# Kernel optimization log

Measured on AMD Instinct MI355X. Metric: run time of the kernel, lower is better.

The kernel has to match this reference:

```python
import jax, jax.numpy as jnp
import numpy as np

B, N, E = 4, 4096, 1024
H, D = 16, 64          # num_heads, head_dim
K = 256                # proj_dim
MAXN = 4096
RANK = 32


def setup_inputs() -> dict:
    key = jax.random.key(0)
    ks = jax.random.split(key, 9)
    def w(k, shape, fan_in):
        return jax.random.normal(k, shape, jnp.float32) * (1.0 / np.sqrt(fan_in))
    return {
        "x": jax.random.normal(ks[0], (B, N, E), jnp.float32),
        "qU": w(ks[1], (RANK, E), E),            # LowRankLinear U: [rank, in]
        "qV": w(ks[2], (E // 2, RANK), RANK),    # LowRankLinear V: [out, rank]
        "qW": w(ks[3], (H * D, E // 2), E // 2), # final query Linear weight
        "qb": jnp.zeros((H * D,), jnp.float32),
        "kW": w(ks[4], (D, E), E),               # key_transform (single kv head)
        "key_proj": w(ks[5], (MAXN, K), MAXN),   # Linformer projection [max_seq_len, proj_dim]
        "oW": w(ks[6], (E, H * D), H * D),
        "ob": jnp.zeros((E,), jnp.float32),
    }


def reference(x, qU, qV, qW, qb, kW, key_proj, oW, ob):
    b, n, _ = x.shape
    # query: LowRankLinear then Linear
    q = ((x @ qU.T) @ qV.T) @ qW.T + qb              # [b, n, H*D]
    # shared single-head key/value, projected along sequence to K slots
    k = x @ kW.T                                     # [b, n, D]
    kv = jnp.einsum('bnd,nk->bkd', k, key_proj[:n])  # [b, K, D]
    q = q.reshape(b, n, H, D).transpose(0, 2, 1, 3)  # [b, H, n, D]
    kv = kv[:, None]                                 # [b, 1, K, D] broadcasts over heads
    scores = jnp.einsum('bhnd,bhkd->bhnk', q, kv) * (D ** -0.5)
    w = jax.nn.softmax(scores, axis=-1)              # [b, H, n, K]
    out = jnp.einsum('bhnk,bhkd->bhnd', w, kv)       # [b, H, n, D]
    out = out.transpose(0, 2, 1, 3).reshape(b, n, H * D)
    return out @ oW.T + ob
```

## Files before the change

### kernel.cpp

```cpp
#include <hip/hip_runtime.h>


typedef unsigned short u16;
typedef _Float16 f16;
typedef __attribute__((ext_vector_type(8))) _Float16 h8;
typedef __attribute__((ext_vector_type(4))) float f32x4;
typedef __attribute__((ext_vector_type(8))) unsigned short us8;
typedef __attribute__((ext_vector_type(4))) unsigned short us4;

__device__ __forceinline__ u16 f2h(float x) {
    f16 h = (f16)x;
    union { f16 hf; u16 u; } c; c.hf = h; return c.u;
}
__device__ __forceinline__ void async16(const void* g, void* l) {
    __builtin_amdgcn_global_load_lds(
        (const __attribute__((address_space(1))) void*)g,
        (__attribute__((address_space(3))) void*)l, 16, 0, 0);
}

__global__ __launch_bounds__(256)
void cvt_w(const float* __restrict__ src, u16* __restrict__ h, int n4) {
    int i = blockIdx.x * 256 + threadIdx.x;
    if (i >= n4) return;
    float4 v = ((const float4*)src)[i];
    u16 hh[4] = {f2h(v.x), f2h(v.y), f2h(v.z), f2h(v.w)};
    ((us4*)h)[i] = *(const us4*)hh;
}

__global__ __launch_bounds__(256)
void wc_compute(const float* __restrict__ qW, const float* __restrict__ qV,
                u16* __restrict__ Wc) {
    __shared__ float Vs[128][32];
    const int t = threadIdx.x;
    const int nl = t >> 3;
    const int rg = t & 7;
    const int n0 = blockIdx.x * 32;
    float acc[4] = {0.f, 0.f, 0.f, 0.f};
    for (int e0 = 0; e0 < 512; e0 += 128) {
#pragma unroll
        for (int u = 0; u < 16; ++u) {
            int idx = u * 256 + t;
            int ee = idx >> 5, rr = idx & 31;
            Vs[ee][rr] = qV[(size_t)(e0 + ee) * 32 + rr];
        }
        __syncthreads();
        for (int e = 0; e < 128; ++e) {
            float w = qW[(size_t)(n0 + nl) * 512 + e0 + e];
#pragma unroll
            for (int rr = 0; rr < 4; ++rr)
                acc[rr] += w * Vs[e][rg * 4 + rr];
        }
        __syncthreads();
    }
#pragma unroll
    for (int rr = 0; rr < 4; ++rr)
        Wc[(size_t)(n0 + nl) * 32 + rg * 4 + rr] = f2h(acc[rr]);
}

template <bool HAS_BIAS, bool OUT_F16>
__global__ __launch_bounds__(256)
void gemm_ps(const u16* __restrict__ A_g, const u16* __restrict__ B_g,
             const float* __restrict__ bias, void* __restrict__ C_p,
             int M, int N, int K) {
    __shared__ u16 LA[128 * 32], LB[128 * 32];
    const int t = threadIdx.x;
    const int wave = t >> 6, lane = t & 63;
    const int l15 = lane & 15, quad = lane >> 4;
    const int wm = (wave >> 1) * 64, wn = (wave & 1) * 64;
    const int gx = gridDim.x;
    const int nwg = gx * gridDim.y;
    const int flat = blockIdx.y * gx + blockIdx.x;
    const int cpx = nwg >> 3;
    const int swz = (flat & 7) * cpx + (flat >> 3);
    const int m0 = (swz / gx) * 128, n0 = (swz % gx) * 128;
    const int rl = lane >> 2, c4 = lane & 3;

    f32x4 acc[4][4] = {};

    for (int k0 = 0; k0 < K; k0 += 32) {
#pragma unroll
        for (int j = 0; j < 2; ++j) {
            const int rloc = (wave * 2 + j) * 16 + rl;
            const size_t ga = (size_t)(m0 + rloc) * K + k0 + c4 * 8;
            const size_t gb = (size_t)(n0 + rloc) * K + k0 + c4 * 8;
            const int lo = (wave * 2 + j) * 512;
            async16(&A_g[ga], &LA[lo]);
            async16(&B_g[gb], &LB[lo]);
        }
        __syncthreads();

        h8 ah[4], bh[4];
#pragma unroll
        for (int i = 0; i < 4; ++i) {
            ah[i] = *(const h8*)&LA[(wm + i * 16 + l15) * 32 + quad * 8];
            bh[i] = *(const h8*)&LB[(wn + i * 16 + l15) * 32 + quad * 8];
        }
#pragma unroll
        for (int i = 0; i < 4; ++i)
#pragma unroll
            for (int j = 0; j < 4; ++j)
                acc[i][j] = __builtin_amdgcn_mfma_f32_16x16x32_f16(ah[i], bh[j], acc[i][j], 0, 0, 0);
        __syncthreads();
    }

#pragma unroll
    for (int j = 0; j < 4; ++j) {
        const int col = n0 + wn + j * 16 + l15;
        const float badd = HAS_BIAS ? bias[col] : 0.f;
#pragma unroll
        for (int i = 0; i < 4; ++i) {
            const int rbase = m0 + wm + i * 16 + quad * 4;
#pragma unroll
            for (int r = 0; r < 4; ++r) {
                float v = acc[i][j][r] + badd;
                size_t idx = (size_t)(rbase + r) * N + col;
                if (OUT_F16) ((u16*)C_p)[idx] = f2h(v);
                else         ((float*)C_p)[idx] = v;
            }
        }
    }
}

__global__ __launch_bounds__(256)
void gemm_x96(const float* __restrict__ A, const u16* __restrict__ B_g,
              u16* __restrict__ t1, float* __restrict__ km, int K) {
    __shared__ u16 Ah[64][40], Bh[96][40];
    const int t = threadIdx.x;
    const int wave = t >> 6, lane = t & 63;
    const int l15 = lane & 15, quad = lane >> 4;
    const int wm = wave * 16;
    const int m0 = blockIdx.y * 64;
    const int arow = t >> 2, acol = (t & 3) * 8;

    f32x4 acc[6] = {};

    for (int k0 = 0; k0 < K; k0 += 32) {
        {
            const float* src = &A[(size_t)(m0 + arow) * K + k0 + acol];
            float4 w0 = ((const float4*)src)[0], w1 = ((const float4*)src)[1];
            float v[8] = {w0.x, w0.y, w0.z, w0.w, w1.x, w1.y, w1.z, w1.w};
            u16 hh[8];
#pragma unroll
            for (int e = 0; e < 8; ++e) hh[e] = f2h(v[e]);
            *(us8*)&Ah[arow][acol] = *(const us8*)&hh[0];
        }
        if (t < 192) {
            const int brow = t >> 1, bcol = (t & 1) * 16;
            size_t base = (size_t)brow * K + k0 + bcol;
            *(us8*)&Bh[brow][bcol]     = *(const us8*)&B_g[base];
            *(us8*)&Bh[brow][bcol + 8] = *(const us8*)&B_g[base + 8];
        }
        __syncthreads();

        h8 ah = *(const h8*)&Ah[wm + l15][quad * 8];
        h8 bh[6];
#pragma unroll
        for (int j = 0; j < 6; ++j)
            bh[j] = *(const h8*)&Bh[j * 16 + l15][quad * 8];
#pragma unroll
        for (int j = 0; j < 6; ++j)
            acc[j] = __builtin_amdgcn_mfma_f32_16x16x32_f16(ah, bh[j], acc[j], 0, 0, 0);
        __syncthreads();
    }

#pragma unroll
    for (int j = 0; j < 6; ++j) {
        const int col96 = j * 16 + l15;
        const int rbase = m0 + wm + quad * 4;
#pragma unroll
        for (int r = 0; r < 4; ++r) {
            float v = acc[j][r];
            const int row = rbase + r;
            if (col96 < 32) t1[(size_t)row * 32 + col96] = f2h(v);
            else            km[(size_t)row * 64 + (col96 - 32)] = v;
        }
    }
}

__global__ __launch_bounds__(256)
void kv_partial(const float* __restrict__ kmat, const float* __restrict__ kp,
                float* __restrict__ part) {
    const int b = blockIdx.y;
    const int seg = blockIdx.z;
    const int kk0 = blockIdx.x * 16;
    const int tid = threadIdx.x;
    const int d = tid & 63, s = tid >> 6;

    float acc[16] = {};
    const int nbeg = seg * 512;
    for (int n = nbeg + s; n < nbeg + 512; n += 4) {
        const float kval = kmat[((size_t)b * 4096 + n) * 64 + d];
        const float* kpr = &kp[(size_t)n * 256 + kk0];
#pragma unroll
        for (int j = 0; j < 16; ++j) acc[j] += kval * kpr[j];
    }
    __shared__ float sm[16][4][64];
#pragma unroll
    for (int j = 0; j < 16; ++j) sm[j][s][d] = acc[j];
    __syncthreads();
    for (int o = tid; o < 16 * 64; o += 256) {
        const int j = o >> 6, dd = o & 63;
        part[(((size_t)seg * 4 + b) * 256 + kk0 + j) * 64 + dd] =
            sm[j][0][dd] + sm[j][1][dd] + sm[j][2][dd] + sm[j][3][dd];
    }
}

__global__ __launch_bounds__(256)
void kv_reduce_cvt(const float* __restrict__ part,
                   u16* __restrict__ kvh, u16* __restrict__ kvTh) {
    const int i = blockIdx.x * 256 + threadIdx.x;
    float s = 0.f;
#pragma unroll
    for (int seg = 0; seg < 8; ++seg) s += part[(size_t)seg * 65536 + i];
    u16 hh = f2h(s);
    kvh[i] = hh;
    const int b = i >> 14, k = (i >> 6) & 255, d = i & 63;
    kvTh[((size_t)b * 64 + d) * 256 + k] = hh;
}

__global__ __launch_bounds__(256)
void attn_fused(const u16* __restrict__ qh,
                const u16* __restrict__ kvh, const u16* __restrict__ kvTh,
                u16* __restrict__ ath) {
    __shared__ u16 Kh_s[64][72];
    __shared__ u16 Vh_s[64][72];
    __shared__ u16 Ps[128 * 64];
    const int b = blockIdx.z, h = blockIdx.y;
    const int t = threadIdx.x, wave = t >> 6, lane = t & 63;
    const int l15 = lane & 15, quad = lane >> 4;
    const int nblk = blockIdx.x * 128;
    const int nwav = wave * 32;
    char* Pb = (char*)Ps;

    h8 Qf[2][2];
#pragma unroll
    for (int nt = 0; nt < 2; ++nt) {
        size_t qoff = ((size_t)(b * 4096 + nblk + nwav + nt * 16 + l15)) * 1024
                      + h * 64 + quad * 8;
#pragma unroll
        for (int c = 0; c < 2; ++c)
            Qf[nt][c] = *(const h8*)&qh[qoff + c * 32];
    }

    f32x4 O[2][4] = {};
    float rsum[2] = {0.f, 0.f};

    const int srow = t >> 3;
    const int scol = (t & 7) * 8;
    const size_t kb = (size_t)b * 16384;

    for (int kc = 0; kc < 4; ++kc) {
        {
            us8 s0 = *(const us8*)&kvh [kb + (size_t)(kc * 64 + srow     ) * 64 + scol];
            us8 s1 = *(const us8*)&kvh [kb + (size_t)(kc * 64 + srow + 32) * 64 + scol];
            us8 s4 = *(const us8*)&kvTh[kb + (size_t)(srow     ) * 256 + kc * 64 + scol];
            us8 s5 = *(const us8*)&kvTh[kb + (size_t)(srow + 32) * 256 + kc * 64 + scol];
            *(us8*)&Kh_s[srow     ][scol] = s0;
            *(us8*)&Kh_s[srow + 32][scol] = s1;
            *(us8*)&Vh_s[srow     ][scol] = s4;
            *(us8*)&Vh_s[srow + 32][scol] = s5;
        }
        __syncthreads();

        f32x4 S[2][4] = {};
#pragma unroll
        for (int ktl = 0; ktl < 4; ++ktl) {
            const int krl = ktl * 16 + l15;
#pragma unroll
            for (int c = 0; c < 2; ++c) {
                h8 Kf = *(const h8*)&Kh_s[krl][c * 32 + quad * 8];
#pragma unroll
                for (int nt = 0; nt < 2; ++nt)
                    S[nt][ktl] = __builtin_amdgcn_mfma_f32_16x16x32_f16(Kf, Qf[nt][c], S[nt][ktl], 0, 0, 0);
            }
        }
#pragma unroll
        for (int nt = 0; nt < 2; ++nt) {
            const int nrel = nwav + nt * 16 + l15;
#pragma unroll
            for (int ktl = 0; ktl < 4; ++ktl) {
                u16 pw[4];
#pragma unroll
                for (int r = 0; r < 4; ++r) {
                    float p = __expf(S[nt][ktl][r] * 0.125f - 4.0f);
                    rsum[nt] += p;
                    pw[r] = f2h(p);
                }
                *(us4*)(Pb + ((nrel * 128 + ktl * 32 + quad * 8) ^ ((nrel & 7) << 4)))
                    = *(const us4*)pw;
            }
        }

#pragma unroll
        for (int c = 0; c < 2; ++c) {
            h8 pf[2];
#pragma unroll
            for (int nt = 0; nt < 2; ++nt) {
                const int nrel = nwav + nt * 16 + l15;
                pf[nt] = *(const h8*)(Pb + ((nrel * 128 + c * 64 + quad * 16) ^ ((nrel & 7) << 4)));
            }
#pragma unroll
            for (int dt = 0; dt < 4; ++dt) {
                const int drow = dt * 16 + l15;
                h8 th = *(const h8*)&Vh_s[drow][c * 32 + quad * 8];
#pragma unroll
                for (int nt = 0; nt < 2; ++nt)
                    O[nt][dt] = __builtin_amdgcn_mfma_f32_16x16x32_f16(pf[nt], th, O[nt][dt], 0, 0, 0);
            }
        }
        __syncthreads();
    }

    float inv[2];
#pragma unroll
    for (int nt = 0; nt < 2; ++nt) {
        float s = rsum[nt];
        s += __shfl_xor(s, 16, 64);
        s += __shfl_xor(s, 32, 64);
        inv[nt] = 1.f / s;
    }

#pragma unroll
    for (int nt = 0; nt < 2; ++nt)
#pragma unroll
        for (int dt = 0; dt < 4; ++dt) {
            const int dcol = dt * 16 + l15;
#pragma unroll
            for (int r = 0; r < 4; ++r) {
                const float qinv = __shfl(inv[nt], quad * 4 + r, 16);
                const int query = nblk + nwav + nt * 16 + quad * 4 + r;
                float v = O[nt][dt][r] * qinv;
                size_t idx = (size_t)(b * 4096 + query) * 1024 + h * 64 + dcol;
                ath[idx] = f2h(v);
            }
        }
}

extern "C" void kernel_launch(void* const* d_in, const int* in_sizes, int n_in,
                              void* d_out, int out_size, void* d_ws, size_t ws_size,
                              hipStream_t stream) {
    const float* x  = (const float*)d_in[0];
    const float* qU = (const float*)d_in[1];
    const float* qV = (const float*)d_in[2];
    const float* qW = (const float*)d_in[3];
    const float* qb = (const float*)d_in[4];
    const float* kW = (const float*)d_in[5];
    const float* kp = (const float*)d_in[6];
    const float* oW = (const float*)d_in[7];
    const float* ob = (const float*)d_in[8];
    float* out = (float*)d_out;

    const int M = 16384;
    u16* W = (u16*)d_ws;
    u16* bUK = W;  W += 98304;
    u16* oWh = W;  W += 1048576;
    u16* WcH = W;  W += 32768;
    u16* t1h = W;  W += 524288;
    u16* qhb = W;  W += 16777216;
    float* km  = (float*)W;  W += 2097152;
    float* part = (float*)W; W += 1048576;
    u16* kvh  = W;  W += 65536;
    u16* kvTh = W;  W += 65536;
    u16* ath = qhb;

    const dim3 blk(256);
    cvt_w<<<dim3(32),   blk, 0, stream>>>(qU, bUK, 8192);
    cvt_w<<<dim3(64),   blk, 0, stream>>>(kW, bUK + 32768, 16384);
    cvt_w<<<dim3(1024), blk, 0, stream>>>(oW, oWh, 262144);
    wc_compute<<<dim3(32), blk, 0, stream>>>(qW, qV, WcH);
    gemm_x96<<<dim3(1, 256), blk, 0, stream>>>(x, bUK, t1h, km, 1024);
    kv_partial<<<dim3(16, 4, 8), blk, 0, stream>>>(km, kp, part);
    kv_reduce_cvt<<<dim3(256), blk, 0, stream>>>(part, kvh, kvTh);
    gemm_ps<true, true><<<dim3(8, 128), blk, 0, stream>>>(
        t1h, WcH, qb, qhb, M, 1024, 32);
    attn_fused<<<dim3(32, 16, 4), blk, 0, stream>>>(qhb, kvh, kvTh, ath);
    gemm_ps<true, false><<<dim3(8, 128), blk, 0, stream>>>(
        ath, oWh, ob, out, M, 1024, 1024);
}
```

Before: 341.8 us.

## Fuse query projection into attention kernel and merge weight prep kernels

The rank-32 query projection (t1 @ Wc^T + bias) is now computed inside the attention kernel with MFMA and staged through shared memory, so the separate GEMM launch and the 32 MB fp16 q buffer write and read go away. The four weight-conversion and Wc kernels are merged into one launch keyed on block index. In exchange, each attention block recomputes its query tile, and the shared memory is now laid out explicitly, with the q staging area sharing space with the K tile.

After: 324.6 us. 5.0% less time.

```diff
diff --git a/kernel.cpp b/kernel.cpp
--- a/kernel.cpp
+++ b/kernel.cpp
@@ -19,42 +19,52 @@
 }
 
 __global__ __launch_bounds__(256)
-void cvt_w(const float* __restrict__ src, u16* __restrict__ h, int n4) {
-    int i = blockIdx.x * 256 + threadIdx.x;
-    if (i >= n4) return;
-    float4 v = ((const float4*)src)[i];
-    u16 hh[4] = {f2h(v.x), f2h(v.y), f2h(v.z), f2h(v.w)};
-    ((us4*)h)[i] = *(const us4*)hh;
-}
-
-__global__ __launch_bounds__(256)
-void wc_compute(const float* __restrict__ qW, const float* __restrict__ qV,
-                u16* __restrict__ Wc) {
+void prep(const float* __restrict__ qU, const float* __restrict__ qV,
+          const float* __restrict__ qW, const float* __restrict__ kW,
+          const float* __restrict__ oW,
+          u16* __restrict__ bUK, u16* __restrict__ oWh, u16* __restrict__ WcH) {
     __shared__ float Vs[128][32];
-    const int t = threadIdx.x;
-    const int nl = t >> 3;
-    const int rg = t & 7;
-    const int n0 = blockIdx.x * 32;
-    float acc[4] = {0.f, 0.f, 0.f, 0.f};
-    for (int e0 = 0; e0 < 512; e0 += 128) {
-#pragma unroll
-        for (int u = 0; u < 16; ++u) {
-            int idx = u * 256 + t;
-            int ee = idx >> 5, rr = idx & 31;
-            Vs[ee][rr] = qV[(size_t)(e0 + ee) * 32 + rr];
-        }
-        __syncthreads();
-        for (int e = 0; e < 128; ++e) {
-            float w = qW[(size_t)(n0 + nl) * 512 + e0 + e];
-#pragma unroll
-            for (int rr = 0; rr < 4; ++rr)
-                acc[rr] += w * Vs[e][rg * 4 + rr];
-        }
-        __syncthreads();
-    }
-#pragma unroll
-    for (int rr = 0; rr < 4; ++rr)
-        Wc[(size_t)(n0 + nl) * 32 + rg * 4 + rr] = f2h(acc[rr]);
+    const int bx = blockIdx.x, t = threadIdx.x;
+    if (bx < 32) {
+        const int nl = t >> 3;
+        const int rg = t & 7;
+        const int n0 = bx * 32;
+        float acc[4] = {0.f, 0.f, 0.f, 0.f};
+        for (int e0 = 0; e0 < 512; e0 += 128) {
+#pragma unroll
+            for (int u = 0; u < 16; ++u) {
+                int idx = u * 256 + t;
+                int ee = idx >> 5, rr = idx & 31;
+                Vs[ee][rr] = qV[(size_t)(e0 + ee) * 32 + rr];
+            }
+            __syncthreads();
+            for (int e = 0; e < 128; ++e) {
+                float w = qW[(size_t)(n0 + nl) * 512 + e0 + e];
+#pragma unroll
+                for (int rr = 0; rr < 4; ++rr)
+                    acc[rr] += w * Vs[e][rg * 4 + rr];
+            }
+            __syncthreads();
+        }
+#pragma unroll
+        for (int rr = 0; rr < 4; ++rr)
+            WcH[(size_t)(n0 + nl) * 32 + rg * 4 + rr] = f2h(acc[rr]);
+    } else if (bx < 64) {
+        int i = (bx - 32) * 256 + t;
+        float4 v = ((const float4*)qU)[i];
+        u16 hh[4] = {f2h(v.x), f2h(v.y), f2h(v.z), f2h(v.w)};
+        ((us4*)bUK)[i] = *(const us4*)hh;
+    } else if (bx < 128) {
+        int i = (bx - 64) * 256 + t;
+        float4 v = ((const float4*)kW)[i];
+        u16 hh[4] = {f2h(v.x), f2h(v.y), f2h(v.z), f2h(v.w)};
+        ((us4*)(bUK + 32768))[i] = *(const us4*)hh;
+    } else {
+        int i = (bx - 128) * 256 + t;
+        float4 v = ((const float4*)oW)[i];
+        u16 hh[4] = {f2h(v.x), f2h(v.y), f2h(v.z), f2h(v.w)};
+        ((us4*)oWh)[i] = *(const us4*)hh;
+    }
 }
 
 template <bool HAS_BIAS, bool OUT_F16>
@@ -219,28 +229,49 @@
 }
 
 __global__ __launch_bounds__(256)
-void attn_fused(const u16* __restrict__ qh,
+void attn_fused(const u16* __restrict__ t1, const u16* __restrict__ WcH,
+                const float* __restrict__ qb,
                 const u16* __restrict__ kvh, const u16* __restrict__ kvTh,
                 u16* __restrict__ ath) {
-    __shared__ u16 Kh_s[64][72];
-    __shared__ u16 Vh_s[64][72];
-    __shared__ u16 Ps[128 * 64];
+    __shared__ __align__(16) char SMEM[34816];
+    u16 (*q_s)[72]  = (u16(*)[72])SMEM;
+    u16 (*Kh_s)[72] = (u16(*)[72])SMEM;
+    u16 (*Vh_s)[72] = (u16(*)[72])(SMEM + 9216);
+    char* Pb        = SMEM + 18432;
+
     const int b = blockIdx.z, h = blockIdx.y;
     const int t = threadIdx.x, wave = t >> 6, lane = t & 63;
     const int l15 = lane & 15, quad = lane >> 4;
     const int nblk = blockIdx.x * 128;
     const int nwav = wave * 32;
-    char* Pb = (char*)Ps;
-
+
+    {
+        h8 ta[2], wb[4];
+#pragma unroll
+        for (int nt = 0; nt < 2; ++nt)
+            ta[nt] = *(const h8*)&t1[(size_t)(b * 4096 + nblk + nwav + nt * 16 + l15) * 32 + quad * 8];
+#pragma unroll
+        for (int j = 0; j < 4; ++j)
+            wb[j] = *(const h8*)&WcH[(size_t)(h * 64 + j * 16 + l15) * 32 + quad * 8];
+#pragma unroll
+        for (int nt = 0; nt < 2; ++nt)
+#pragma unroll
+            for (int j = 0; j < 4; ++j) {
+                f32x4 qa = {};
+                qa = __builtin_amdgcn_mfma_f32_16x16x32_f16(ta[nt], wb[j], qa, 0, 0, 0);
+                const float badd = qb[h * 64 + j * 16 + l15];
+#pragma unroll
+                for (int r = 0; r < 4; ++r)
+                    q_s[nwav + nt * 16 + quad * 4 + r][j * 16 + l15] = f2h(qa[r] + badd);
+            }
+    }
     h8 Qf[2][2];
 #pragma unroll
-    for (int nt = 0; nt < 2; ++nt) {
-        size_t qoff = ((size_t)(b * 4096 + nblk + nwav + nt * 16 + l15)) * 1024
-                      + h * 64 + quad * 8;
+    for (int nt = 0; nt < 2; ++nt)
 #pragma unroll
         for (int c = 0; c < 2; ++c)
-            Qf[nt][c] = *(const h8*)&qh[qoff + c * 32];
-    }
+            Qf[nt][c] = *(const h8*)&q_s[nwav + nt * 16 + l15][c * 32 + quad * 8];
+    __syncthreads();
 
     f32x4 O[2][4] = {};
     float rsum[2] = {0.f, 0.f};
@@ -356,24 +387,18 @@
     u16* oWh = W;  W += 1048576;
     u16* WcH = W;  W += 32768;
     u16* t1h = W;  W += 524288;
-    u16* qhb = W;  W += 16777216;
+    u16* ath = W;  W += 16777216;
     float* km  = (float*)W;  W += 2097152;
     float* part = (float*)W; W += 1048576;
     u16* kvh  = W;  W += 65536;
     u16* kvTh = W;  W += 65536;
-    u16* ath = qhb;
 
     const dim3 blk(256);
-    cvt_w<<<dim3(32),   blk, 0, stream>>>(qU, bUK, 8192);
-    cvt_w<<<dim3(64),   blk, 0, stream>>>(kW, bUK + 32768, 16384);
-    cvt_w<<<dim3(1024), blk, 0, stream>>>(oW, oWh, 262144);
-    wc_compute<<<dim3(32), blk, 0, stream>>>(qW, qV, WcH);
+    prep<<<dim3(1152), blk, 0, stream>>>(qU, qV, qW, kW, oW, bUK, oWh, WcH);
     gemm_x96<<<dim3(1, 256), blk, 0, stream>>>(x, bUK, t1h, km, 1024);
     kv_partial<<<dim3(16, 4, 8), blk, 0, stream>>>(km, kp, part);
     kv_reduce_cvt<<<dim3(256), blk, 0, stream>>>(part, kvh, kvTh);
-    gemm_ps<true, true><<<dim3(8, 128), blk, 0, stream>>>(
-        t1h, WcH, qb, qhb, M, 1024, 32);
-    attn_fused<<<dim3(32, 16, 4), blk, 0, stream>>>(qhb, kvh, kvTh, ath);
+    attn_fused<<<dim3(32, 16, 4), blk, 0, stream>>>(t1h, WcH, qb, kvh, kvTh, ath);
     gemm_ps<true, false><<<dim3(8, 128), blk, 0, stream>>>(
         ath, oWh, ob, out, M, 1024, 1024);
 }
```
